# Optimization experiments

Measured on AMD Instinct MI355X. Metric: run time of the kernel, lower is better.

The kernel has to match this reference:

```python
import jax, jax.numpy as jnp
import numpy as np

B, NP, C, H, NCURVES = 128, 196, 768, 12, 6
N = NP + 1  # +1 cls token


def setup_inputs() -> dict:
    key = jax.random.key(0)
    k0, k1, k2, k3, k4 = jax.random.split(key, 5)
    x = jax.random.normal(k0, (B, N, C), dtype=jnp.float32)
    w_qkv = jax.random.normal(k1, (3 * C, C), dtype=jnp.float32) * 0.02
    w_proj = jax.random.normal(k2, (C, C), dtype=jnp.float32) * 0.02
    b_proj = jnp.zeros((C,), dtype=jnp.float32)
    ai = jax.random.normal(k3, (NCURVES, H), dtype=jnp.float32)
    # per-curve inverse space-filling-curve index permutations of [0, NP)
    curve_idx = jnp.stack([
        jax.random.permutation(jax.random.fold_in(k4, c), NP)
        for c in range(NCURVES)
    ]).astype(jnp.int32)
    return {"x": x, "w_qkv": w_qkv, "w_proj": w_proj, "b_proj": b_proj,
            "ai": ai, "curve_idx": curve_idx}


def _decay_mask(ai, curve_idx, n, dtype):
    # ai: [NC, H]; curve_idx: [NC, NP] permutations; returns averaged mask [H, n, n]
    idx = jnp.arange(n)
    E = jnp.abs(idx[:, None] - idx[None, :]).astype(dtype)  # [n, n]
    p = jax.nn.sigmoid(ai)                                   # [NC, H]
    Mfull = p[:, :, None, None] ** E[None, None]             # [NC, H, n, n]
    gather = lambda m, ind: m[:, ind][:, :, ind]             # m: [H, n, n] -> [H, NP, NP]
    Mg = jax.vmap(gather)(Mfull, curve_idx)                  # [NC, H, NP, NP]
    # re-attach cls row/col of ones
    Mpad = jnp.ones((Mg.shape[0], Mg.shape[1], n, n), dtype).at[:, :, 1:, 1:].set(Mg)
    return Mpad.mean(axis=0)                                 # [H, n, n]


def reference(x, w_qkv, w_proj, b_proj, ai, curve_idx):
    b, n, c = x.shape
    nc, h = ai.shape
    hd = c // h
    scale = hd ** -0.5
    qkv = (x @ w_qkv.T).reshape(b, n, 3, h, hd).transpose(2, 0, 3, 1, 4)
    q, k, v = qkv[0], qkv[1], qkv[2]                         # [b, h, n, hd]
    attn = jnp.einsum('bhnd,bhmd->bhnm', q, k) * scale       # [b, h, n, n]
    M = _decay_mask(ai, curve_idx, n, x.dtype)               # [h, n, n]
    attn = jax.nn.softmax(attn * M[None], axis=-1)
    out = jnp.einsum('bhnm,bhmd->bhnd', attn, v)
    out = out.transpose(0, 2, 1, 3).reshape(b, n, c)
    return out @ w_proj.T + b_proj
```

## Files before the change

kernel.cpp:

```cpp
#include <hip/hip_runtime.h>
#include <hip/hip_bf16.h>
#include <stdint.h>

#define TOK   25216
#define CC    768
#define HH    12
#define NKV   224
#define BHN   1536

typedef __attribute__((ext_vector_type(8))) __bf16 bf16x8;
typedef __attribute__((ext_vector_type(4))) float  f32x4;

__device__ __forceinline__ ushort f2bf(float f) {
  union { float f; uint32_t u; } v; v.f = f;
  uint32_t u = v.u;
  u += 0x7FFFu + ((u >> 16) & 1u);
  return (ushort)(u >> 16);
}
__device__ __forceinline__ float bf2f(ushort s) {
  union { uint32_t u; float f; } v; v.u = ((uint32_t)s) << 16; return v.f;
}

__device__ __forceinline__ void gload_lds16(const void* g, void* l) {
  __builtin_amdgcn_global_load_lds(
      (const __attribute__((address_space(1))) unsigned int*)g,
      (__attribute__((address_space(3))) unsigned int*)l, 16, 0, 0);
}

__global__ __launch_bounds__(256) void conv_bf16(const float* __restrict__ in,
                                                 ushort* __restrict__ out, int n) {
  int idx = (blockIdx.x * 256 + threadIdx.x) * 4;
  if (idx < n) {
    float4 v = *(const float4*)(in + idx);
    ushort4 o;
    o.x = f2bf(v.x); o.y = f2bf(v.y); o.z = f2bf(v.z); o.w = f2bf(v.w);
    *(ushort4*)(out + idx) = o;
  }
}

__global__ __launch_bounds__(256) void mask_kernel(const float* __restrict__ ai,
                                                   const int* __restrict__ ci,
                                                   ushort* __restrict__ Mb) {
  int h = blockIdx.x / NKV;
  int i = blockIdx.x % NKV;
  int j = threadIdx.x;
  if (j >= NKV) return;
  float val;
  if (j >= 197)      val = 0.f;
  else if (i >= 197) val = 1.f;
  else if (i == 0 || j == 0) val = 1.f;
  else {
    float acc = 0.f;
#pragma unroll
    for (int c = 0; c < 6; ++c) {
      float a  = ai[c * 12 + h];
      float p  = 1.f / (1.f + expf(-a));
      float l2 = log2f(p);
      int   e  = ci[c * 196 + i - 1] - ci[c * 196 + j - 1];
      if (e < 0) e = -e;
      acc += exp2f(l2 * (float)e);
    }
    val = acc * (1.f / 6.f);
  }
  Mb[((size_t)h * NKV + i) * NKV + j] = f2bf(val);
}

template <int EPI, int NT>
__global__ __launch_bounds__(256) void gemm128(
    const ushort* __restrict__ A, const ushort* __restrict__ Bw,
    ushort* __restrict__ Qb, ushort* __restrict__ Kb, ushort* __restrict__ Vtb,
    const float* __restrict__ bias, float* __restrict__ outp) {
  __shared__ alignas(16) char As[128 * 128];
  __shared__ alignas(16) char Bs[128 * 128];
  const int tid = threadIdx.x;
  const int lane = tid & 63, wid = tid >> 6;
  const int g = lane >> 4, li = lane & 15;
  const int m0 = (blockIdx.x / NT) * 128;
  const int n0 = (blockIdx.x % NT) * 128;
  const int wr = wid >> 1, wc = wid & 1;

  f32x4 acc[4][4];
  f32x4 zero = {0.f, 0.f, 0.f, 0.f};
#pragma unroll
  for (int i = 0; i < 4; ++i)
#pragma unroll
    for (int j = 0; j < 4; ++j) acc[i][j] = zero;

  for (int kk = 0; kk < 768; kk += 64) {
#pragma unroll
    for (int p = 0; p < 4; ++p) {
      int o = tid * 16 + p * 4096;
      int row = o >> 7;
      int cs = (o & 127) ^ ((row & 7) << 4);
      gload_lds16(A + (size_t)(m0 + row) * 768 + kk + (cs >> 1), As + o);
      gload_lds16(Bw + (size_t)(n0 + row) * 768 + kk + (cs >> 1), Bs + o);
    }
    __syncthreads();
#pragma unroll
    for (int ks = 0; ks < 2; ++ks) {
      bf16x8 af[4], bfr[4];
#pragma unroll
      for (int mt = 0; mt < 4; ++mt) {
        int row = wr * 64 + mt * 16 + li;
        int c = (ks * 64 + g * 16) ^ ((row & 7) << 4);
        af[mt] = *(const bf16x8*)(As + row * 128 + c);
      }
#pragma unroll
      for (int nt = 0; nt < 4; ++nt) {
        int row = wc * 64 + nt * 16 + li;
        int c = (ks * 64 + g * 16) ^ ((row & 7) << 4);
        bfr[nt] = *(const bf16x8*)(Bs + row * 128 + c);
      }
#pragma unroll
      for (int mt = 0; mt < 4; ++mt)
#pragma unroll
        for (int nt = 0; nt < 4; ++nt)
          acc[mt][nt] = __builtin_amdgcn_mfma_f32_16x16x32_bf16(
              af[mt], bfr[nt], acc[mt][nt], 0, 0, 0);
    }
    __syncthreads();
  }

  if (EPI == 0) {
    const int s3 = n0 / 768;
#pragma unroll
    for (int nt = 0; nt < 4; ++nt) {
      int n = n0 + wc * 64 + nt * 16 + li;
      int rem = n - s3 * 768;
      int hh = rem >> 6, d = rem & 63;
#pragma unroll
      for (int mt = 0; mt < 4; ++mt) {
#pragma unroll
        for (int r = 0; r < 4; ++r) {
          int m = m0 + wr * 64 + mt * 16 + 4 * g + r;
          uint32_t bI = ((uint32_t)m * 85164u) >> 24;
          int tok = m - (int)bI * 197;
          ushort val = f2bf(acc[mt][nt][r]);
          size_t bh = (size_t)bI * 12 + hh;
          if (s3 == 0)      Qb[(bh * NKV + tok) * 64 + d] = val;
          else if (s3 == 1) Kb[(bh * NKV + tok) * 64 + d] = val;
          else              Vtb[(bh * 64 + d) * NKV + tok] = val;
        }
      }
    }
  } else {
#pragma unroll
    for (int nt = 0; nt < 4; ++nt) {
      int n = n0 + wc * 64 + nt * 16 + li;
      float bv = bias[n];
#pragma unroll
      for (int mt = 0; mt < 4; ++mt) {
#pragma unroll
        for (int r = 0; r < 4; ++r) {
          int m = m0 + wr * 64 + mt * 16 + 4 * g + r;
          outp[(size_t)m * 768 + n] = acc[mt][nt][r] + bv;
        }
      }
    }
  }
}

#define KL_S 72
#define VL_S 232
__global__ __launch_bounds__(448) void attn_kernel(
    const ushort* __restrict__ Qb, const ushort* __restrict__ Kb,
    const ushort* __restrict__ Vtb, const ushort* __restrict__ Mb,
    ushort* __restrict__ Ob) {
  __shared__ alignas(16) ushort Kl[NKV * KL_S];
  __shared__ alignas(16) ushort Vl[64 * VL_S];
  __shared__ alignas(16) ushort Pl[7 * 16 * VL_S];
  const int tid = threadIdx.x, lane = tid & 63, wid = tid >> 6;
  const int g = lane >> 4, li = lane & 15;
  const int bh = blockIdx.x;
  const int b = bh / 12, h = bh % 12;

  const ushort* Kg = Kb + (size_t)bh * (NKV * 64);
  const ushort* Vg = Vtb + (size_t)bh * (64 * NKV);
  const ushort* Qg = Qb + (size_t)bh * (NKV * 64);

#pragma unroll
  for (int p = 0; p < 4; ++p) {
    int o = (tid + p * 448) * 16;
    int row = o >> 7, c = o & 127;
    *(bf16x8*)((char*)Kl + row * 144 + c) = *(const bf16x8*)((const char*)Kg + o);
  }
#pragma unroll
  for (int p = 0; p < 4; ++p) {
    int o = (tid + p * 448) * 16;
    int row = o / 448, c = o % 448;
    *(bf16x8*)((char*)Vl + row * 464 + c) = *(const bf16x8*)((const char*)Vg + o);
  }
  __syncthreads();

  for (int t = 0; t < 2; ++t) {
    int rt = wid * 2 + t;
    int r0 = rt * 16;
    if (r0 >= 197) continue;
    bf16x8 qf[2];
#pragma unroll
    for (int ks = 0; ks < 2; ++ks)
      qf[ks] = *(const bf16x8*)(Qg + (size_t)(r0 + li) * 64 + ks * 32 + g * 8);

    f32x4 acc[14];
#pragma unroll
    for (int ct = 0; ct < 14; ++ct) {
      bf16x8 kf0 = *(const bf16x8*)((const char*)Kl + (ct * 16 + li) * 144 + g * 16);
      bf16x8 kf1 = *(const bf16x8*)((const char*)Kl + (ct * 16 + li) * 144 + 64 + g * 16);
      f32x4 z = {0.f, 0.f, 0.f, 0.f};
      z = __builtin_amdgcn_mfma_f32_16x16x32_bf16(kf0, qf[0], z, 0, 0, 0);
      acc[ct] = __builtin_amdgcn_mfma_f32_16x16x32_bf16(kf1, qf[1], z, 0, 0, 0);
    }

    int ig = r0 + li;
    const ushort* Mrow = Mb + ((size_t)h * NKV + ig) * NKV;
    float mx = -3e38f;
#pragma unroll
    for (int ct = 0; ct < 14; ++ct) {
      int j0 = ct * 16 + 4 * g;
      ushort4 mv = *(const ushort4*)(Mrow + j0);
#pragma unroll
      for (int r = 0; r < 4; ++r) {
        float Lv = (j0 + r < 197)
                     ? acc[ct][r] * 0.125f * bf2f(((const ushort*)&mv)[r])
                     : -1e30f;
        acc[ct][r] = Lv;
        mx = fmaxf(mx, Lv);
      }
    }
    mx = fmaxf(mx, __shfl_xor(mx, 16));
    mx = fmaxf(mx, __shfl_xor(mx, 32));

    float sum = 0.f;
    ushort* Prow = Pl + ((size_t)wid * 16 + li) * VL_S;
#pragma unroll
    for (int ct = 0; ct < 14; ++ct) {
      ushort4 pv;
#pragma unroll
      for (int r = 0; r < 4; ++r) {
        float p = exp2f((acc[ct][r] - mx) * 1.44269504f);
        sum += p;
        ((ushort*)&pv)[r] = f2bf(p);
      }
      *(ushort4*)(Prow + ct * 16 + 4 * g) = pv;
    }
    sum += __shfl_xor(sum, 16);
    sum += __shfl_xor(sum, 32);

    asm volatile("s_waitcnt lgkmcnt(0)" ::: "memory");
    __builtin_amdgcn_sched_barrier(0);

    f32x4 oacc[4];
#pragma unroll
    for (int dt = 0; dt < 4; ++dt) oacc[dt] = (f32x4){0.f, 0.f, 0.f, 0.f};
    const ushort* Pbase = Pl + (size_t)wid * 16 * VL_S;
#pragma unroll
    for (int ks = 0; ks < 7; ++ks) {
      bf16x8 pf = *(const bf16x8*)(Pbase + (size_t)li * VL_S + ks * 32 + g * 8);
#pragma unroll
      for (int dt = 0; dt < 4; ++dt) {
        bf16x8 vf = *(const bf16x8*)(Vl + (size_t)(dt * 16 + li) * VL_S + ks * 32 + g * 8);
        oacc[dt] = __builtin_amdgcn_mfma_f32_16x16x32_bf16(pf, vf, oacc[dt], 0, 0, 0);
      }
    }
    float inv[4];
#pragma unroll
    for (int r = 0; r < 4; ++r) {
      float sr = __shfl(sum, 4 * g + r);
      inv[r] = 1.f / sr;
    }
#pragma unroll
    for (int dt = 0; dt < 4; ++dt) {
      int d = dt * 16 + li;
#pragma unroll
      for (int r = 0; r < 4; ++r) {
        int tokn = r0 + 4 * g + r;
        if (tokn < 197) {
          size_t rowi = (size_t)b * 197 + tokn;
          Ob[rowi * 768 + h * 64 + d] = f2bf(oacc[dt][r] * inv[r]);
        }
      }
    }
  }
}

extern "C" void kernel_launch(void* const* d_in, const int* in_sizes, int n_in,
                              void* d_out, int out_size, void* d_ws, size_t ws_size,
                              hipStream_t stream) {
  const float* x      = (const float*)d_in[0];
  const float* w_qkv  = (const float*)d_in[1];
  const float* w_proj = (const float*)d_in[2];
  const float* b_proj = (const float*)d_in[3];
  const float* ai     = (const float*)d_in[4];
  const int*   ci     = (const int*)d_in[5];
  float* out = (float*)d_out;

  ushort* x_bf    = (ushort*)d_ws;
  ushort* wqkv_bf = x_bf + (size_t)TOK * CC;
  ushort* wproj_bf= wqkv_bf + (size_t)2304 * CC;
  ushort* Qb      = wproj_bf + (size_t)CC * CC;
  ushort* Kb      = Qb + (size_t)BHN * NKV * 64;
  ushort* Vtb     = Kb + (size_t)BHN * NKV * 64;
  ushort* Mb      = Vtb + (size_t)BHN * NKV * 64;
  ushort* Ob      = x_bf;

  conv_bf16<<<(TOK * CC / 4 + 255) / 256, 256, 0, stream>>>(x, x_bf, TOK * CC);
  conv_bf16<<<(2304 * CC / 4 + 255) / 256, 256, 0, stream>>>(w_qkv, wqkv_bf, 2304 * CC);
  conv_bf16<<<(CC * CC / 4 + 255) / 256, 256, 0, stream>>>(w_proj, wproj_bf, CC * CC);
  mask_kernel<<<12 * NKV, 256, 0, stream>>>(ai, ci, Mb);
  gemm128<0, 18><<<197 * 18, 256, 0, stream>>>(x_bf, wqkv_bf, Qb, Kb, Vtb, nullptr, nullptr);
  attn_kernel<<<BHN, 448, 0, stream>>>(Qb, Kb, Vtb, Mb, Ob);
  gemm128<1, 6><<<197 * 6, 256, 0, stream>>>(Ob, wproj_bf, nullptr, nullptr, nullptr, b_proj, out);
}
```

Before: 467.6 us.

## Store V untransposed, transpose in LDS, read K from global, remap workgroups per XCD

The QKV GEMM epilogue now writes V in the same token-major layout as Q and K, replacing the strided transposed store. The attention kernel transposes V into LDS on load, drops the K shared-memory tile and reads K fragments directly from global/L2, and adds a min-blocks-per-CU hint of 4. Both GEMM launches remap block indices so that consecutive tiles land on the same XCD for better L2 locality. The scalar transposing LDS stores may cause bank conflicts, and uncached K reads add global traffic per wave.

```diff
diff --git a/kernel.cpp b/kernel.cpp
--- a/kernel.cpp
+++ b/kernel.cpp
@@ -9,6 +9,7 @@
 #define BHN   1536
 
 typedef __attribute__((ext_vector_type(8))) __bf16 bf16x8;
+typedef __attribute__((ext_vector_type(8))) ushort u16x8;
 typedef __attribute__((ext_vector_type(4))) float  f32x4;
 
 __device__ __forceinline__ ushort f2bf(float f) {
@@ -68,15 +69,18 @@
 template <int EPI, int NT>
 __global__ __launch_bounds__(256) void gemm128(
     const ushort* __restrict__ A, const ushort* __restrict__ Bw,
-    ushort* __restrict__ Qb, ushort* __restrict__ Kb, ushort* __restrict__ Vtb,
-    const float* __restrict__ bias, float* __restrict__ outp) {
+    ushort* __restrict__ Qb, ushort* __restrict__ Kb, ushort* __restrict__ Vb,
+    const float* __restrict__ bias, float* __restrict__ outp, int nwg) {
   __shared__ alignas(16) char As[128 * 128];
   __shared__ alignas(16) char Bs[128 * 128];
   const int tid = threadIdx.x;
   const int lane = tid & 63, wid = tid >> 6;
   const int g = lane >> 4, li = lane & 15;
-  const int m0 = (blockIdx.x / NT) * 128;
-  const int n0 = (blockIdx.x % NT) * 128;
+  const int q8 = nwg >> 3, r8 = nwg & 7;
+  const int xcd = blockIdx.x & 7, sidx = blockIdx.x >> 3;
+  const int wgid = (xcd < r8 ? xcd * (q8 + 1) : r8 * (q8 + 1) + (xcd - r8) * q8) + sidx;
+  const int m0 = (wgid / NT) * 128;
+  const int n0 = (wgid % NT) * 128;
   const int wr = wid >> 1, wc = wid & 1;
 
   f32x4 acc[4][4];
@@ -123,6 +127,7 @@
 
   if (EPI == 0) {
     const int s3 = n0 / 768;
+    ushort* dst = (s3 == 0) ? Qb : (s3 == 1) ? Kb : Vb;
 #pragma unroll
     for (int nt = 0; nt < 4; ++nt) {
       int n = n0 + wc * 64 + nt * 16 + li;
@@ -135,11 +140,8 @@
           int m = m0 + wr * 64 + mt * 16 + 4 * g + r;
           uint32_t bI = ((uint32_t)m * 85164u) >> 24;
           int tok = m - (int)bI * 197;
-          ushort val = f2bf(acc[mt][nt][r]);
           size_t bh = (size_t)bI * 12 + hh;
-          if (s3 == 0)      Qb[(bh * NKV + tok) * 64 + d] = val;
-          else if (s3 == 1) Kb[(bh * NKV + tok) * 64 + d] = val;
-          else              Vtb[(bh * 64 + d) * NKV + tok] = val;
+          dst[(bh * NKV + tok) * 64 + d] = f2bf(acc[mt][nt][r]);
         }
       }
     }
@@ -160,13 +162,11 @@
   }
 }
 
-#define KL_S 72
 #define VL_S 232
-__global__ __launch_bounds__(448) void attn_kernel(
+__global__ __launch_bounds__(448, 4) void attn_kernel(
     const ushort* __restrict__ Qb, const ushort* __restrict__ Kb,
-    const ushort* __restrict__ Vtb, const ushort* __restrict__ Mb,
+    const ushort* __restrict__ Vb, const ushort* __restrict__ Mb,
     ushort* __restrict__ Ob) {
-  __shared__ alignas(16) ushort Kl[NKV * KL_S];
   __shared__ alignas(16) ushort Vl[64 * VL_S];
   __shared__ alignas(16) ushort Pl[7 * 16 * VL_S];
   const int tid = threadIdx.x, lane = tid & 63, wid = tid >> 6;
@@ -175,20 +175,18 @@
   const int b = bh / 12, h = bh % 12;
 
   const ushort* Kg = Kb + (size_t)bh * (NKV * 64);
-  const ushort* Vg = Vtb + (size_t)bh * (64 * NKV);
+  const ushort* Vg = Vb + (size_t)bh * (NKV * 64);
   const ushort* Qg = Qb + (size_t)bh * (NKV * 64);
 
 #pragma unroll
   for (int p = 0; p < 4; ++p) {
     int o = (tid + p * 448) * 16;
-    int row = o >> 7, c = o & 127;
-    *(bf16x8*)((char*)Kl + row * 144 + c) = *(const bf16x8*)((const char*)Kg + o);
-  }
-#pragma unroll
-  for (int p = 0; p < 4; ++p) {
-    int o = (tid + p * 448) * 16;
-    int row = o / 448, c = o % 448;
-    *(bf16x8*)((char*)Vl + row * 464 + c) = *(const bf16x8*)((const char*)Vg + o);
+    int tok = o >> 7;
+    int d0 = (o >> 1) & 63;
+    u16x8 v = *(const u16x8*)((const char*)Vg + o);
+#pragma unroll
+    for (int j = 0; j < 8; ++j)
+      Vl[(d0 + j) * VL_S + tok] = v[j];
   }
   __syncthreads();
 
@@ -204,8 +202,8 @@
     f32x4 acc[14];
 #pragma unroll
     for (int ct = 0; ct < 14; ++ct) {
-      bf16x8 kf0 = *(const bf16x8*)((const char*)Kl + (ct * 16 + li) * 144 + g * 16);
-      bf16x8 kf1 = *(const bf16x8*)((const char*)Kl + (ct * 16 + li) * 144 + 64 + g * 16);
+      bf16x8 kf0 = *(const bf16x8*)(Kg + (size_t)(ct * 16 + li) * 64 + g * 8);
+      bf16x8 kf1 = *(const bf16x8*)(Kg + (size_t)(ct * 16 + li) * 64 + 32 + g * 8);
       f32x4 z = {0.f, 0.f, 0.f, 0.f};
       z = __builtin_amdgcn_mfma_f32_16x16x32_bf16(kf0, qf[0], z, 0, 0, 0);
       acc[ct] = __builtin_amdgcn_mfma_f32_16x16x32_bf16(kf1, qf[1], z, 0, 0, 0);
@@ -299,15 +297,15 @@
   ushort* wproj_bf= wqkv_bf + (size_t)2304 * CC;
   ushort* Qb      = wproj_bf + (size_t)CC * CC;
   ushort* Kb      = Qb + (size_t)BHN * NKV * 64;
-  ushort* Vtb     = Kb + (size_t)BHN * NKV * 64;
-  ushort* Mb      = Vtb + (size_t)BHN * NKV * 64;
+  ushort* Vb      = Kb + (size_t)BHN * NKV * 64;
+  ushort* Mb      = Vb + (size_t)BHN * NKV * 64;
   ushort* Ob      = x_bf;
 
   conv_bf16<<<(TOK * CC / 4 + 255) / 256, 256, 0, stream>>>(x, x_bf, TOK * CC);
   conv_bf16<<<(2304 * CC / 4 + 255) / 256, 256, 0, stream>>>(w_qkv, wqkv_bf, 2304 * CC);
   conv_bf16<<<(CC * CC / 4 + 255) / 256, 256, 0, stream>>>(w_proj, wproj_bf, CC * CC);
   mask_kernel<<<12 * NKV, 256, 0, stream>>>(ai, ci, Mb);
-  gemm128<0, 18><<<197 * 18, 256, 0, stream>>>(x_bf, wqkv_bf, Qb, Kb, Vtb, nullptr, nullptr);
-  attn_kernel<<<BHN, 448, 0, stream>>>(Qb, Kb, Vtb, Mb, Ob);
-  gemm128<1, 6><<<197 * 6, 256, 0, stream>>>(Ob, wproj_bf, nullptr, nullptr, nullptr, b_proj, out);
-}
+  gemm128<0, 18><<<197 * 18, 256, 0, stream>>>(x_bf, wqkv_bf, Qb, Kb, Vb, nullptr, nullptr, 197 * 18);
+  attn_kernel<<<BHN, 448, 0, stream>>>(Qb, Kb, Vb, Mb, Ob);
+  gemm128<1, 6><<<197 * 6, 256, 0, stream>>>(Ob, wproj_bf, nullptr, nullptr, nullptr, b_proj, out, 197 * 6);
+}
```

Measured after the change: 476.9 us. 2.0% more time.
